# Kernel tuning notes

Hardware: AMD Instinct MI355X
Metric: run time of the kernel (lower is better)

## Reference

```python
import jax, jax.numpy as jnp
import numpy as np

MARGIN = 0.2
SCALE = 30.0
EPS_NORM = 1e-12
EPS_COS = 1e-7

B, D, C = 4096, 256, 5994


def setup_inputs() -> dict:
    key = jax.random.key(0)
    kx, kw, kl = jax.random.split(key, 3)
    x = jax.random.normal(kx, (B, D), dtype=jnp.float32)
    # xavier_normal_ init: std = sqrt(2 / (fan_in + fan_out))
    w_std = np.sqrt(2.0 / (D + C)).astype(np.float32)
    W = jax.random.normal(kw, (D, C), dtype=jnp.float32) * w_std
    label = jax.random.randint(kl, (B,), 0, C, dtype=jnp.int64)
    return {"x": x, "W": W, "label": label}


def reference(x, W, label):
    # L2-normalize rows of x and columns of W
    xn = x / jnp.clip(jnp.linalg.norm(x, axis=1, keepdims=True), EPS_NORM)
    wn = W / jnp.clip(jnp.linalg.norm(W, axis=0, keepdims=True), EPS_NORM)
    # cosine similarity logits [B, C]
    costh = xn @ wn
    # faithful clamp (note: original clamps upper bound to 1+eps)
    costh = jnp.clip(costh, -1.0 + EPS_COS, 1.0 + EPS_COS)
    theta = jnp.arccos(costh)
    costh_m = jnp.cos(theta + MARGIN)
    # apply margin only on the target class, then scale
    one_hot = jnp.arange(costh.shape[1])[None, :] == label[:, None]  # [B, C] bool
    output = jnp.where(one_hot, costh_m, costh) * SCALE
    # cross entropy (mean over batch)
    logp = jax.nn.log_softmax(output, axis=-1)
    loss = -jnp.mean(jnp.take_along_axis(logp, label[:, None], axis=1))
    # top-1 accuracy in percent
    acc = jnp.mean((jnp.argmax(output, axis=-1) == label).astype(jnp.float32)) * 100.0
    return loss, acc
```

## Files before the change

### kernel.cpp

```cpp
#include <hip/hip_runtime.h>
#include <hip/hip_bf16.h>

#define BB 4096
#define DD 256
#define CC 5994
#define CPAD 6144
#define NCHUNK 384
#define PARTS 16
#define NSUB 12
#define COSM 0.9800665778412416f
#define SINM 0.19866933079506122f

typedef __attribute__((ext_vector_type(8))) short bf16x8;
typedef __attribute__((ext_vector_type(4))) float f32x4;

__device__ __forceinline__ unsigned short f2bf(float f) {
  union { float f; unsigned u; } v; v.f = f;
  unsigned r = v.u + 0x7fffu + ((v.u >> 16) & 1u);
  return (unsigned short)(r >> 16);
}

__global__ void k_xnorm(const float* __restrict__ x, unsigned short* __restrict__ xnS) {
  int tgi = threadIdx.x >> 6, l = threadIdx.x & 63;
  int row = blockIdx.x * 4 + tgi;
  float4 v = reinterpret_cast<const float4*>(x + (size_t)row * DD)[l];
  float ss = v.x * v.x + v.y * v.y + v.z * v.z + v.w * v.w;
#pragma unroll
  for (int m = 32; m >= 1; m >>= 1) ss += __shfl_xor(ss, m, 64);
  float inv = 1.0f / fmaxf(sqrtf(ss), 1e-12f);
  ushort4 o;
  o.x = f2bf(v.x * inv); o.y = f2bf(v.y * inv);
  o.z = f2bf(v.z * inv); o.w = f2bf(v.w * inv);
  int off = (row >> 4) * 4096 + (l >> 3) * 512 + ((l >> 1) & 3) * 128 + (row & 15) * 8 + (l & 1) * 4;
  *reinterpret_cast<ushort4*>(xnS + off) = o;
}

__global__ void k_wnorm(const float* __restrict__ W, unsigned short* __restrict__ wnS) {
  __shared__ float pp[16][17];
  __shared__ float sinv[16];
  int t = threadIdx.x;
  int lr = t & 15, u = t >> 4;
  int chunk = blockIdx.x;
  int c = chunk * 16 + lr;
  int D0 = u * 16;
  float v[16];
  float ss = 0.f;
#pragma unroll
  for (int i = 0; i < 16; ++i) {
    float xv = (c < CC) ? W[(size_t)(D0 + i) * CC + c] : 0.f;
    v[i] = xv; ss += xv * xv;
  }
  pp[u][lr] = ss;
  __syncthreads();
  if (t < 16) {
    float tot = 0.f;
#pragma unroll
    for (int g = 0; g < 16; ++g) tot += pp[g][t];
    sinv[t] = (chunk * 16 + t < CC) ? 1.0f / fmaxf(sqrtf(tot), 1e-12f) : 0.f;
  }
  __syncthreads();
  float inv = sinv[lr];
  int base = chunk * 4096 + (u >> 1) * 512 + ((2 * u) & 3) * 128 + lr * 8;
  unsigned wds[4];
#pragma unroll
  for (int q = 0; q < 4; ++q)
    wds[q] = (unsigned)f2bf(v[2 * q] * inv) | ((unsigned)f2bf(v[2 * q + 1] * inv) << 16);
  *reinterpret_cast<uint4*>(wnS + base) = make_uint4(wds[0], wds[1], wds[2], wds[3]);
#pragma unroll
  for (int q = 0; q < 4; ++q)
    wds[q] = (unsigned)f2bf(v[8 + 2 * q] * inv) | ((unsigned)f2bf(v[9 + 2 * q] * inv) << 16);
  *reinterpret_cast<uint4*>(wnS + base + 128) = make_uint4(wds[0], wds[1], wds[2], wds[3]);
}

__launch_bounds__(256, 2)
__global__ void k_main(const unsigned short* __restrict__ xnS,
                       const unsigned short* __restrict__ wnS,
                       const int* __restrict__ label,
                       float* __restrict__ sp, float* __restrict__ vmp,
                       float* __restrict__ vtp) {
  __shared__ uint4 ldsB[2][1024];
  int bid = blockIdx.x;
  int sw = (bid & 7) * 64 + (bid >> 3);
  int part = sw >> 5;
  int rowblk = sw & 31;
  int t = threadIdx.x, w = t >> 6, l = t & 63;
  int lg = l >> 4, lr = l & 15;
  int r0 = rowblk * 128 + w * 32;

  bf16x8 a[2][8];
#pragma unroll
  for (int rt = 0; rt < 2; ++rt) {
    const unsigned short* ap = xnS + ((r0 >> 4) + rt) * 4096 + lg * 128 + lr * 8;
#pragma unroll
    for (int ks = 0; ks < 8; ++ks)
      a[rt][ks] = *reinterpret_cast<const bf16x8*>(ap + ks * 512);
  }
  int lab[8];
#pragma unroll
  for (int rt = 0; rt < 2; ++rt)
#pragma unroll
    for (int j = 0; j < 4; ++j) lab[rt * 4 + j] = label[r0 + rt * 16 + lg * 4 + j];

  float s[8], vm[8], vt[8];
#pragma unroll
  for (int i = 0; i < 8; ++i) { s[i] = 0.f; vm[i] = -2.f; vt[i] = -2.f; }

  const uint4* gbase = reinterpret_cast<const uint4*>(wnS + (size_t)part * NSUB * 8192);
  {
    uint4 p0 = gbase[t], p1 = gbase[t + 256], p2 = gbase[t + 512], p3 = gbase[t + 768];
    ldsB[0][t] = p0; ldsB[0][t + 256] = p1; ldsB[0][t + 512] = p2; ldsB[0][t + 768] = p3;
  }
  __syncthreads();

  for (int it = 0; it < NSUB; ++it) {
    uint4 n0, n1, n2, n3;
    bool pf = (it + 1 < NSUB);
    if (pf) {
      const uint4* g = gbase + (it + 1) * 1024;
      n0 = g[t]; n1 = g[t + 256]; n2 = g[t + 512]; n3 = g[t + 768];
    }
    const unsigned short* lb = reinterpret_cast<const unsigned short*>(&ldsB[it & 1][0]);
#pragma unroll
    for (int c2 = 0; c2 < 2; ++c2) {
      bf16x8 b[8];
#pragma unroll
      for (int ks = 0; ks < 8; ++ks)
        b[ks] = *reinterpret_cast<const bf16x8*>(lb + c2 * 4096 + ks * 512 + l * 8);
      f32x4 acc[2] = {{0.f, 0.f, 0.f, 0.f}, {0.f, 0.f, 0.f, 0.f}};
#pragma unroll
      for (int ks = 0; ks < 8; ++ks) {
        acc[0] = __builtin_amdgcn_mfma_f32_16x16x32_bf16(a[0][ks], b[ks], acc[0], 0, 0, 0);
        acc[1] = __builtin_amdgcn_mfma_f32_16x16x32_bf16(a[1][ks], b[ks], acc[1], 0, 0, 0);
      }
      int col = part * 384 + it * 32 + c2 * 16 + lr;
#pragma unroll
      for (int rt = 0; rt < 2; ++rt)
#pragma unroll
        for (int j = 0; j < 4; ++j) {
          float v = acc[rt][j];
          s[rt * 4 + j] += __expf(__builtin_fmaf(v, 30.f, -30.f));
          bool ist = (col == lab[rt * 4 + j]);
          vt[rt * 4 + j] = ist ? v : vt[rt * 4 + j];
          vm[rt * 4 + j] = fmaxf(vm[rt * 4 + j], ist ? -2.f : v);
        }
    }
    if (pf) {
      uint4* d = &ldsB[(it + 1) & 1][0];
      d[t] = n0; d[t + 256] = n1; d[t + 512] = n2; d[t + 768] = n3;
    }
    __syncthreads();
  }

#pragma unroll
  for (int i = 0; i < 8; ++i) {
#pragma unroll
    for (int mk = 1; mk < 16; mk <<= 1) {
      s[i] += __shfl_xor(s[i], mk, 64);
      vm[i] = fmaxf(vm[i], __shfl_xor(vm[i], mk, 64));
      vt[i] = fmaxf(vt[i], __shfl_xor(vt[i], mk, 64));
    }
    if (lr == 0) {
      int row = r0 + (i >> 2) * 16 + lg * 4 + (i & 3);
      int idx = row * PARTS + part;
      sp[idx] = s[i]; vmp[idx] = vm[i]; vtp[idx] = vt[i];
    }
  }
}

__global__ void k_combine(const float* __restrict__ sp, const float* __restrict__ vmp,
                          const float* __restrict__ vtp, float* __restrict__ accum) {
  int t = threadIdx.x;
  int row = blockIdx.x * 256 + t;
  float4 s4a[4], m4a[4], t4a[4];
#pragma unroll
  for (int q = 0; q < 4; ++q) {
    s4a[q] = reinterpret_cast<const float4*>(sp + row * PARTS)[q];
    m4a[q] = reinterpret_cast<const float4*>(vmp + row * PARTS)[q];
    t4a[q] = reinterpret_cast<const float4*>(vtp + row * PARTS)[q];
  }
  float s = 0.f, vm = -2.f, vt = -2.f;
#pragma unroll
  for (int q = 0; q < 4; ++q) {
    s += s4a[q].x + s4a[q].y + s4a[q].z + s4a[q].w;
    vm = fmaxf(vm, fmaxf(fmaxf(m4a[q].x, m4a[q].y), fmaxf(m4a[q].z, m4a[q].w)));
    vt = fmaxf(vt, fmaxf(fmaxf(t4a[q].x, t4a[q].y), fmaxf(t4a[q].z, t4a[q].w)));
  }
  float vtc = fminf(fmaxf(vt, -1.f + 1e-7f), 1.f + 1e-7f);
  float sn = sqrtf(fmaxf(1.f - vtc * vtc, 0.f));
  float tg = 30.f * (vtc * COSM - sn * SINM);
  float sadj = s - __expf(30.f * vt - 30.f) + __expf(tg - 30.f);
  float loss = 30.f + logf(sadj) - tg;
  float corr = (tg >= 30.f * vm) ? 1.f : 0.f;
#pragma unroll
  for (int mk = 32; mk >= 1; mk >>= 1) {
    loss += __shfl_xor(loss, mk, 64);
    corr += __shfl_xor(corr, mk, 64);
  }
  __shared__ float ls[4], cs[4];
  if ((t & 63) == 0) { ls[t >> 6] = loss; cs[t >> 6] = corr; }
  __syncthreads();
  if (t == 0) {
    atomicAdd(accum + 0, ls[0] + ls[1] + ls[2] + ls[3]);
    atomicAdd(accum + 1, cs[0] + cs[1] + cs[2] + cs[3]);
  }
}

__global__ void k_final(const float* __restrict__ accum, float* __restrict__ out) {
  out[0] = accum[0] / (float)BB;
  out[1] = accum[1] * (100.0f / (float)BB);
}

extern "C" void kernel_launch(void* const* d_in, const int* in_sizes, int n_in,
                              void* d_out, int out_size, void* d_ws, size_t ws_size,
                              hipStream_t stream) {
  const float* x = (const float*)d_in[0];
  const float* W = (const float*)d_in[1];
  const int* label = (const int*)d_in[2];
  float* out = (float*)d_out;

  char* ws = (char*)d_ws;
  unsigned short* wnS = (unsigned short*)(ws);
  unsigned short* xnS = (unsigned short*)(ws + 3145728);
  size_t po = 5242880;
  float* sp  = (float*)(ws + po);
  float* vmp = (float*)(ws + po + 262144);
  float* vtp = (float*)(ws + po + 524288);
  float* accum = (float*)(ws + po + 786432);

  hipMemsetAsync(accum, 0, 8, stream);
  k_xnorm<<<BB / 4, 256, 0, stream>>>(x, xnS);
  k_wnorm<<<NCHUNK, 256, 0, stream>>>(W, wnS);
  k_main<<<512, 256, 0, stream>>>(xnS, wnS, label, sp, vmp, vtp);
  k_combine<<<BB / 256, 256, 0, stream>>>(sp, vmp, vtp, accum);
  k_final<<<1, 1, 0, stream>>>(accum, out);
}
```

Measured before the change: 43.68 us.

## Fuse prep kernels and tail kernels, double the W tile per pipeline stage

Merges the x and W normalization kernels into one launch that also zeroes the accumulator, which removes the memset. The combine and final kernels become one tail kernel that uses a ticket counter so the last block writes the outputs. The main GEMM stage now stages 64 columns per iteration (6 iterations instead of 12) with a doubled LDS buffer. This cuts launch count and barrier overhead, at the cost of more LDS and more registers per block, which may lower occupancy.

```diff
diff --git a/kernel.cpp b/kernel.cpp
--- a/kernel.cpp
+++ b/kernel.cpp
@@ -7,7 +7,7 @@
 #define CPAD 6144
 #define NCHUNK 384
 #define PARTS 16
-#define NSUB 12
+#define NSUB 6
 #define COSM 0.9800665778412416f
 #define SINM 0.19866933079506122f
 
@@ -20,56 +20,60 @@
   return (unsigned short)(r >> 16);
 }
 
-__global__ void k_xnorm(const float* __restrict__ x, unsigned short* __restrict__ xnS) {
-  int tgi = threadIdx.x >> 6, l = threadIdx.x & 63;
-  int row = blockIdx.x * 4 + tgi;
-  float4 v = reinterpret_cast<const float4*>(x + (size_t)row * DD)[l];
-  float ss = v.x * v.x + v.y * v.y + v.z * v.z + v.w * v.w;
-#pragma unroll
-  for (int m = 32; m >= 1; m >>= 1) ss += __shfl_xor(ss, m, 64);
-  float inv = 1.0f / fmaxf(sqrtf(ss), 1e-12f);
-  ushort4 o;
-  o.x = f2bf(v.x * inv); o.y = f2bf(v.y * inv);
-  o.z = f2bf(v.z * inv); o.w = f2bf(v.w * inv);
-  int off = (row >> 4) * 4096 + (l >> 3) * 512 + ((l >> 1) & 3) * 128 + (row & 15) * 8 + (l & 1) * 4;
-  *reinterpret_cast<ushort4*>(xnS + off) = o;
-}
-
-__global__ void k_wnorm(const float* __restrict__ W, unsigned short* __restrict__ wnS) {
-  __shared__ float pp[16][17];
-  __shared__ float sinv[16];
+__global__ void k_prep(const float* __restrict__ x, const float* __restrict__ W,
+                       unsigned short* __restrict__ xnS, unsigned short* __restrict__ wnS,
+                       unsigned* __restrict__ accum) {
+  int b = blockIdx.x;
   int t = threadIdx.x;
-  int lr = t & 15, u = t >> 4;
-  int chunk = blockIdx.x;
-  int c = chunk * 16 + lr;
-  int D0 = u * 16;
-  float v[16];
-  float ss = 0.f;
-#pragma unroll
-  for (int i = 0; i < 16; ++i) {
-    float xv = (c < CC) ? W[(size_t)(D0 + i) * CC + c] : 0.f;
-    v[i] = xv; ss += xv * xv;
-  }
-  pp[u][lr] = ss;
-  __syncthreads();
-  if (t < 16) {
-    float tot = 0.f;
-#pragma unroll
-    for (int g = 0; g < 16; ++g) tot += pp[g][t];
-    sinv[t] = (chunk * 16 + t < CC) ? 1.0f / fmaxf(sqrtf(tot), 1e-12f) : 0.f;
-  }
-  __syncthreads();
-  float inv = sinv[lr];
-  int base = chunk * 4096 + (u >> 1) * 512 + ((2 * u) & 3) * 128 + lr * 8;
-  unsigned wds[4];
-#pragma unroll
-  for (int q = 0; q < 4; ++q)
-    wds[q] = (unsigned)f2bf(v[2 * q] * inv) | ((unsigned)f2bf(v[2 * q + 1] * inv) << 16);
-  *reinterpret_cast<uint4*>(wnS + base) = make_uint4(wds[0], wds[1], wds[2], wds[3]);
-#pragma unroll
-  for (int q = 0; q < 4; ++q)
-    wds[q] = (unsigned)f2bf(v[8 + 2 * q] * inv) | ((unsigned)f2bf(v[9 + 2 * q] * inv) << 16);
-  *reinterpret_cast<uint4*>(wnS + base + 128) = make_uint4(wds[0], wds[1], wds[2], wds[3]);
+  if (b < 1024) {
+    int tgi = t >> 6, l = t & 63;
+    int row = b * 4 + tgi;
+    float4 v = reinterpret_cast<const float4*>(x + (size_t)row * DD)[l];
+    float ss = v.x * v.x + v.y * v.y + v.z * v.z + v.w * v.w;
+#pragma unroll
+    for (int m = 32; m >= 1; m >>= 1) ss += __shfl_xor(ss, m, 64);
+    float inv = 1.0f / fmaxf(sqrtf(ss), 1e-12f);
+    ushort4 o;
+    o.x = f2bf(v.x * inv); o.y = f2bf(v.y * inv);
+    o.z = f2bf(v.z * inv); o.w = f2bf(v.w * inv);
+    int off = (row >> 4) * 4096 + (l >> 3) * 512 + ((l >> 1) & 3) * 128 + (row & 15) * 8 + (l & 1) * 4;
+    *reinterpret_cast<ushort4*>(xnS + off) = o;
+  } else {
+    if (b == 1024 && t < 4) accum[t] = 0u;
+    __shared__ float pp[16][17];
+    __shared__ float sinv[16];
+    int lr = t & 15, u = t >> 4;
+    int chunk = b - 1024;
+    int c = chunk * 16 + lr;
+    int D0 = u * 16;
+    float v[16];
+    float ss = 0.f;
+#pragma unroll
+    for (int i = 0; i < 16; ++i) {
+      float xv = (c < CC) ? W[(size_t)(D0 + i) * CC + c] : 0.f;
+      v[i] = xv; ss += xv * xv;
+    }
+    pp[u][lr] = ss;
+    __syncthreads();
+    if (t < 16) {
+      float tot = 0.f;
+#pragma unroll
+      for (int g = 0; g < 16; ++g) tot += pp[g][t];
+      sinv[t] = (chunk * 16 + t < CC) ? 1.0f / fmaxf(sqrtf(tot), 1e-12f) : 0.f;
+    }
+    __syncthreads();
+    float inv = sinv[lr];
+    int base = chunk * 4096 + (u >> 1) * 512 + ((2 * u) & 3) * 128 + lr * 8;
+    unsigned wds[4];
+#pragma unroll
+    for (int q = 0; q < 4; ++q)
+      wds[q] = (unsigned)f2bf(v[2 * q] * inv) | ((unsigned)f2bf(v[2 * q + 1] * inv) << 16);
+    *reinterpret_cast<uint4*>(wnS + base) = make_uint4(wds[0], wds[1], wds[2], wds[3]);
+#pragma unroll
+    for (int q = 0; q < 4; ++q)
+      wds[q] = (unsigned)f2bf(v[8 + 2 * q] * inv) | ((unsigned)f2bf(v[9 + 2 * q] * inv) << 16);
+    *reinterpret_cast<uint4*>(wnS + base + 128) = make_uint4(wds[0], wds[1], wds[2], wds[3]);
+  }
 }
 
 __launch_bounds__(256, 2)
@@ -78,7 +82,7 @@
                        const int* __restrict__ label,
                        float* __restrict__ sp, float* __restrict__ vmp,
                        float* __restrict__ vtp) {
-  __shared__ uint4 ldsB[2][1024];
+  __shared__ uint4 ldsB[2][2048];
   int bid = blockIdx.x;
   int sw = (bid & 7) * 64 + (bid >> 3);
   int part = sw >> 5;
@@ -105,48 +109,51 @@
 #pragma unroll
   for (int i = 0; i < 8; ++i) { s[i] = 0.f; vm[i] = -2.f; vt[i] = -2.f; }
 
-  const uint4* gbase = reinterpret_cast<const uint4*>(wnS + (size_t)part * NSUB * 8192);
+  const uint4* gbase = reinterpret_cast<const uint4*>(wnS) + (size_t)part * 6144;
   {
-    uint4 p0 = gbase[t], p1 = gbase[t + 256], p2 = gbase[t + 512], p3 = gbase[t + 768];
-    ldsB[0][t] = p0; ldsB[0][t + 256] = p1; ldsB[0][t + 512] = p2; ldsB[0][t + 768] = p3;
+#pragma unroll
+    for (int i = 0; i < 8; ++i) ldsB[0][t + i * 256] = gbase[t + i * 256];
   }
   __syncthreads();
 
   for (int it = 0; it < NSUB; ++it) {
-    uint4 n0, n1, n2, n3;
+    uint4 nx[8];
     bool pf = (it + 1 < NSUB);
     if (pf) {
-      const uint4* g = gbase + (it + 1) * 1024;
-      n0 = g[t]; n1 = g[t + 256]; n2 = g[t + 512]; n3 = g[t + 768];
+      const uint4* g = gbase + (it + 1) * 2048;
+#pragma unroll
+      for (int i = 0; i < 8; ++i) nx[i] = g[t + i * 256];
     }
     const unsigned short* lb = reinterpret_cast<const unsigned short*>(&ldsB[it & 1][0]);
 #pragma unroll
-    for (int c2 = 0; c2 < 2; ++c2) {
-      bf16x8 b[8];
+    for (int c4 = 0; c4 < 4; ++c4) {
+      bf16x8 bfr[8];
 #pragma unroll
       for (int ks = 0; ks < 8; ++ks)
-        b[ks] = *reinterpret_cast<const bf16x8*>(lb + c2 * 4096 + ks * 512 + l * 8);
-      f32x4 acc[2] = {{0.f, 0.f, 0.f, 0.f}, {0.f, 0.f, 0.f, 0.f}};
+        bfr[ks] = *reinterpret_cast<const bf16x8*>(lb + c4 * 4096 + ks * 512 + l * 8);
+      f32x4 acc0 = {0.f, 0.f, 0.f, 0.f}, acc1 = {0.f, 0.f, 0.f, 0.f};
 #pragma unroll
       for (int ks = 0; ks < 8; ++ks) {
-        acc[0] = __builtin_amdgcn_mfma_f32_16x16x32_bf16(a[0][ks], b[ks], acc[0], 0, 0, 0);
-        acc[1] = __builtin_amdgcn_mfma_f32_16x16x32_bf16(a[1][ks], b[ks], acc[1], 0, 0, 0);
+        acc0 = __builtin_amdgcn_mfma_f32_16x16x32_bf16(a[0][ks], bfr[ks], acc0, 0, 0, 0);
+        acc1 = __builtin_amdgcn_mfma_f32_16x16x32_bf16(a[1][ks], bfr[ks], acc1, 0, 0, 0);
       }
-      int col = part * 384 + it * 32 + c2 * 16 + lr;
-#pragma unroll
-      for (int rt = 0; rt < 2; ++rt)
-#pragma unroll
-        for (int j = 0; j < 4; ++j) {
-          float v = acc[rt][j];
-          s[rt * 4 + j] += __expf(__builtin_fmaf(v, 30.f, -30.f));
-          bool ist = (col == lab[rt * 4 + j]);
-          vt[rt * 4 + j] = ist ? v : vt[rt * 4 + j];
-          vm[rt * 4 + j] = fmaxf(vm[rt * 4 + j], ist ? -2.f : v);
-        }
+      int col = part * 384 + it * 64 + c4 * 16 + lr;
+#pragma unroll
+      for (int j = 0; j < 4; ++j) {
+        float v0 = acc0[j], v1 = acc1[j];
+        s[j]     += __expf(__builtin_fmaf(v0, 30.f, -30.f));
+        s[4 + j] += __expf(__builtin_fmaf(v1, 30.f, -30.f));
+        bool i0 = (col == lab[j]), i1 = (col == lab[4 + j]);
+        vt[j]     = i0 ? v0 : vt[j];
+        vt[4 + j] = i1 ? v1 : vt[4 + j];
+        vm[j]     = fmaxf(vm[j],     i0 ? -2.f : v0);
+        vm[4 + j] = fmaxf(vm[4 + j], i1 ? -2.f : v1);
+      }
     }
     if (pf) {
       uint4* d = &ldsB[(it + 1) & 1][0];
-      d[t] = n0; d[t + 256] = n1; d[t + 512] = n2; d[t + 768] = n3;
+#pragma unroll
+      for (int i = 0; i < 8; ++i) d[t + i * 256] = nx[i];
     }
     __syncthreads();
   }
@@ -167,23 +174,20 @@
   }
 }
 
-__global__ void k_combine(const float* __restrict__ sp, const float* __restrict__ vmp,
-                          const float* __restrict__ vtp, float* __restrict__ accum) {
+__global__ void k_tail(const float* __restrict__ sp, const float* __restrict__ vmp,
+                       const float* __restrict__ vtp, float* __restrict__ accum,
+                       float* __restrict__ out) {
   int t = threadIdx.x;
-  int row = blockIdx.x * 256 + t;
-  float4 s4a[4], m4a[4], t4a[4];
+  int row = blockIdx.x * 64 + t;
+  float s = 0.f, vm = -2.f, vt = -2.f;
 #pragma unroll
   for (int q = 0; q < 4; ++q) {
-    s4a[q] = reinterpret_cast<const float4*>(sp + row * PARTS)[q];
-    m4a[q] = reinterpret_cast<const float4*>(vmp + row * PARTS)[q];
-    t4a[q] = reinterpret_cast<const float4*>(vtp + row * PARTS)[q];
-  }
-  float s = 0.f, vm = -2.f, vt = -2.f;
-#pragma unroll
-  for (int q = 0; q < 4; ++q) {
-    s += s4a[q].x + s4a[q].y + s4a[q].z + s4a[q].w;
-    vm = fmaxf(vm, fmaxf(fmaxf(m4a[q].x, m4a[q].y), fmaxf(m4a[q].z, m4a[q].w)));
-    vt = fmaxf(vt, fmaxf(fmaxf(t4a[q].x, t4a[q].y), fmaxf(t4a[q].z, t4a[q].w)));
+    float4 aq = reinterpret_cast<const float4*>(sp + row * PARTS)[q];
+    float4 mq = reinterpret_cast<const float4*>(vmp + row * PARTS)[q];
+    float4 tq = reinterpret_cast<const float4*>(vtp + row * PARTS)[q];
+    s += aq.x + aq.y + aq.z + aq.w;
+    vm = fmaxf(vm, fmaxf(fmaxf(mq.x, mq.y), fmaxf(mq.z, mq.w)));
+    vt = fmaxf(vt, fmaxf(fmaxf(tq.x, tq.y), fmaxf(tq.z, tq.w)));
   }
   float vtc = fminf(fmaxf(vt, -1.f + 1e-7f), 1.f + 1e-7f);
   float sn = sqrtf(fmaxf(1.f - vtc * vtc, 0.f));
@@ -196,18 +200,18 @@
     loss += __shfl_xor(loss, mk, 64);
     corr += __shfl_xor(corr, mk, 64);
   }
-  __shared__ float ls[4], cs[4];
-  if ((t & 63) == 0) { ls[t >> 6] = loss; cs[t >> 6] = corr; }
-  __syncthreads();
   if (t == 0) {
-    atomicAdd(accum + 0, ls[0] + ls[1] + ls[2] + ls[3]);
-    atomicAdd(accum + 1, cs[0] + cs[1] + cs[2] + cs[3]);
-  }
-}
-
-__global__ void k_final(const float* __restrict__ accum, float* __restrict__ out) {
-  out[0] = accum[0] / (float)BB;
-  out[1] = accum[1] * (100.0f / (float)BB);
+    atomicAdd(accum + 0, loss);
+    atomicAdd(accum + 1, corr);
+    __threadfence();
+    unsigned ticket = atomicAdd(reinterpret_cast<unsigned*>(accum) + 2, 1u);
+    if (ticket == 63) {
+      float L = atomicAdd(accum + 0, 0.0f);
+      float Cr = atomicAdd(accum + 1, 0.0f);
+      out[0] = L / (float)BB;
+      out[1] = Cr * (100.0f / (float)BB);
+    }
+  }
 }
 
 extern "C" void kernel_launch(void* const* d_in, const int* in_sizes, int n_in,
@@ -227,10 +231,7 @@
   float* vtp = (float*)(ws + po + 524288);
   float* accum = (float*)(ws + po + 786432);
 
-  hipMemsetAsync(accum, 0, 8, stream);
-  k_xnorm<<<BB / 4, 256, 0, stream>>>(x, xnS);
-  k_wnorm<<<NCHUNK, 256, 0, stream>>>(W, wnS);
+  k_prep<<<1408, 256, 0, stream>>>(x, W, xnS, wnS, (unsigned*)accum);
   k_main<<<512, 256, 0, stream>>>(xnS, wnS, label, sp, vmp, vtp);
-  k_combine<<<BB / 256, 256, 0, stream>>>(sp, vmp, vtp, accum);
-  k_final<<<1, 1, 0, stream>>>(accum, out);
-}
+  k_tail<<<BB / 64, 64, 0, stream>>>(sp, vmp, vtp, accum, out);
+}
```

Result: slower. 51.10 us (+17.0%).
